# Kernel tuning notes

Measured on AMD Instinct MI355X. Metric: run time of the kernel, lower is better.

Reference implementation:

```python
import jax, jax.numpy as jnp
import numpy as np

B, H, W, C, WS, SHIFT, NH = 64, 14, 14, 1024, 7, 3, 32
HD = C // NH
SCALE = HD ** -0.5

def _rel_index():
    coords = np.stack(np.meshgrid(np.arange(WS), np.arange(WS), indexing='ij'))  # [2,ws,ws]
    flat = coords.reshape(2, -1)
    rel = (flat[:, :, None] - flat[:, None, :]).transpose(1, 2, 0)  # [49,49,2]
    rel[:, :, 0] += WS - 1
    rel[:, :, 1] += WS - 1
    rel[:, :, 0] *= 2 * WS - 1
    return jnp.asarray(rel.sum(-1))  # [49,49] int

REL_IDX = _rel_index()

def _shift_mask():
    m = np.zeros((H, W), np.float32)
    cnt = 0
    for hs in (slice(0, -WS), slice(-WS, -SHIFT), slice(-SHIFT, None)):
        for ws_ in (slice(0, -WS), slice(-WS, -SHIFT), slice(-SHIFT, None)):
            m[hs, ws_] = cnt
            cnt += 1
    mw = m.reshape(H // WS, WS, W // WS, WS).transpose(0, 2, 1, 3).reshape(-1, WS * WS)
    diff = mw[:, None, :] - mw[:, :, None]
    return jnp.asarray(np.where(diff != 0, -100.0, 0.0).astype(np.float32))  # [nW,49,49]

ATTN_MASK = _shift_mask()

def layernorm(x, g, b, eps=1e-5):
    mu = x.mean(-1, keepdims=True)
    var = ((x - mu) ** 2).mean(-1, keepdims=True)
    return (x - mu) * jax.lax.rsqrt(var + eps) * g + b

def window_partition(x):  # [B,H,W,C] -> [B*nW, 49, C]
    x = x.reshape(B, H // WS, WS, W // WS, WS, C)
    return x.transpose(0, 1, 3, 2, 4, 5).reshape(-1, WS * WS, C)

def window_reverse(x):  # [B*nW, 49, C] -> [B,H,W,C]
    x = x.reshape(B, H // WS, W // WS, WS, WS, C)
    return x.transpose(0, 1, 3, 2, 4, 5).reshape(B, H, W, C)

def swin_block(x, p, shift):
    (ln1_g, ln1_b, qkv_w, qkv_b, rpb, proj_w, proj_b,
     ln2_g, ln2_b, fc1_w, fc1_b, fc2_w, fc2_b) = p
    h = layernorm(x, ln1_g, ln1_b).reshape(B, H, W, C)
    if shift:
        h = jnp.roll(h, (-SHIFT, -SHIFT), axis=(1, 2))
    hw = window_partition(h)                              # [Bn,49,C]
    qkv = hw @ qkv_w + qkv_b                              # [Bn,49,3C]
    q, k, v = qkv.reshape(-1, WS * WS, 3, NH, HD).transpose(2, 0, 3, 1, 4)  # each [Bn,NH,49,HD]
    attn = jnp.einsum('bhqd,bhkd->bhqk', q * SCALE, k)    # [Bn,NH,49,49]
    attn = attn + rpb[REL_IDX].transpose(2, 0, 1)[None]   # fused rel-pos bias
    if shift:
        nW = ATTN_MASK.shape[0]
        attn = attn.reshape(B, nW, NH, WS * WS, WS * WS) + ATTN_MASK[None, :, None]
        attn = attn.reshape(-1, NH, WS * WS, WS * WS)
    attn = jax.nn.softmax(attn, axis=-1)
    o = jnp.einsum('bhqk,bhkd->bhqd', attn, v).transpose(0, 2, 1, 3).reshape(-1, WS * WS, C)
    o = o @ proj_w + proj_b
    o = window_reverse(o)
    if shift:
        o = jnp.roll(o, (SHIFT, SHIFT), axis=(1, 2))
    x = x + o.reshape(B, H * W, C)
    h2 = layernorm(x, ln2_g, ln2_b)
    return x + jax.nn.gelu(h2 @ fc1_w + fc1_b, approximate=False) @ fc2_w + fc2_b

def setup_inputs() -> dict:
    key = jax.random.key(0)
    ks = iter(jax.random.split(key, 64))
    def rnd(shape, s=0.02):
        return jax.random.normal(next(ks), shape, jnp.float32) * s
    inp = {'x': jax.random.normal(next(ks), (B, H * W, C), jnp.float32)}
    for i in range(2):
        inp[f'b{i}_ln1_g'] = jnp.ones((C,), jnp.float32)
        inp[f'b{i}_ln1_b'] = jnp.zeros((C,), jnp.float32)
        inp[f'b{i}_qkv_w'] = rnd((C, 3 * C))
        inp[f'b{i}_qkv_b'] = jnp.zeros((3 * C,), jnp.float32)
        inp[f'b{i}_rpb'] = rnd(((2 * WS - 1) ** 2, NH))
        inp[f'b{i}_proj_w'] = rnd((C, C))
        inp[f'b{i}_proj_b'] = jnp.zeros((C,), jnp.float32)
        inp[f'b{i}_ln2_g'] = jnp.ones((C,), jnp.float32)
        inp[f'b{i}_ln2_b'] = jnp.zeros((C,), jnp.float32)
        inp[f'b{i}_fc1_w'] = rnd((C, 4 * C))
        inp[f'b{i}_fc1_b'] = jnp.zeros((4 * C,), jnp.float32)
        inp[f'b{i}_fc2_w'] = rnd((4 * C, C))
        inp[f'b{i}_fc2_b'] = jnp.zeros((C,), jnp.float32)
    inp['h_ln_g'] = jnp.ones((C,), jnp.float32)
    inp['h_ln_b'] = jnp.zeros((C,), jnp.float32)
    inp['h_w1'] = rnd((C, 512)); inp['h_b1'] = jnp.zeros((512,), jnp.float32)
    inp['h_w2'] = rnd((512, 128)); inp['h_b2'] = jnp.zeros((128,), jnp.float32)
    inp['h_w3'] = rnd((128, 2)); inp['h_b3'] = jnp.zeros((2,), jnp.float32)
    return inp

def reference(x,
              b0_ln1_g, b0_ln1_b, b0_qkv_w, b0_qkv_b, b0_rpb, b0_proj_w, b0_proj_b,
              b0_ln2_g, b0_ln2_b, b0_fc1_w, b0_fc1_b, b0_fc2_w, b0_fc2_b,
              b1_ln1_g, b1_ln1_b, b1_qkv_w, b1_qkv_b, b1_rpb, b1_proj_w, b1_proj_b,
              b1_ln2_g, b1_ln2_b, b1_fc1_w, b1_fc1_b, b1_fc2_w, b1_fc2_b,
              h_ln_g, h_ln_b, h_w1, h_b1, h_w2, h_b2, h_w3, h_b3):
    p0 = (b0_ln1_g, b0_ln1_b, b0_qkv_w, b0_qkv_b, b0_rpb, b0_proj_w, b0_proj_b,
          b0_ln2_g, b0_ln2_b, b0_fc1_w, b0_fc1_b, b0_fc2_w, b0_fc2_b)
    p1 = (b1_ln1_g, b1_ln1_b, b1_qkv_w, b1_qkv_b, b1_rpb, b1_proj_w, b1_proj_b,
          b1_ln2_g, b1_ln2_b, b1_fc1_w, b1_fc1_b, b1_fc2_w, b1_fc2_b)
    x = swin_block(x, p0, shift=False)
    x = swin_block(x, p1, shift=True)
    pooled = x.mean(axis=1)  # global avg pool -> [B, C]
    h = layernorm(pooled, h_ln_g, h_ln_b)
    h = jax.nn.gelu(h @ h_w1 + h_b1, approximate=False)  # dropout is identity (eval)
    h = jax.nn.gelu(h @ h_w2 + h_b2, approximate=False)
    return h @ h_w3 + h_b3  # [B, num_classes]
```

## Files before the change

kernel.cpp:

```cpp
#include <hip/hip_runtime.h>
#include <hip/hip_bf16.h>
#include <hip/hip_fp16.h>
#include <math.h>

#define BB 64
#define CC 1024
#define NH 32
#define NTOK (BB * 14 * 14)
#define SCALE 0.17677669529663687f

typedef __attribute__((ext_vector_type(8))) short short8;
typedef __attribute__((ext_vector_type(8))) unsigned short us8;
typedef __attribute__((ext_vector_type(4))) float f32x4;

__device__ __align__(16) float  g_X  [(size_t)NTOK * CC];
__device__ __align__(16) unsigned short g_Qh[(size_t)NTOK * 3072];
__device__ __align__(16) unsigned short g_B[(size_t)NTOK * CC];
__device__ __align__(16) unsigned short g_C[(size_t)NTOK * 4096];
__device__ __align__(16) unsigned short g_Wq[(size_t)2*3072*1024];
__device__ __align__(16) unsigned short g_Wp[(size_t)2*1024*1024];
__device__ __align__(16) unsigned short g_W1[(size_t)2*4096*1024];
__device__ __align__(16) unsigned short g_W2[(size_t)2*1024*4096];
__device__ __align__(16) float g_H0[64 * CC];
__device__ __align__(16) float g_H1[64 * 512];
__device__ __align__(16) float g_H2[64 * 128];

__device__ __forceinline__ float gelu_f(float x) {
    return 0.5f * x * (1.0f + erff(x * 0.70710678118654752f));
}

__device__ __forceinline__ unsigned short f16_bits(float v) {
    _Float16 hh = (_Float16)v;
    return *(unsigned short*)&hh;
}
__device__ __forceinline__ float f16_val(unsigned short u) {
    _Float16 h;
    __builtin_memcpy(&h, &u, 2);
    return (float)h;
}

__device__ __forceinline__ int win_to_xrow(int r, int shifted) {
    int bn = r / 49, t = r - bn * 49;
    int b = bn >> 2, w = bn & 3;
    int wh = w >> 1, ww_ = w & 1;
    int th = t / 7, tw = t - th * 7;
    int gh = wh * 7 + th, gw = ww_ * 7 + tw;
    if (shifted) { gh = gh + 3; if (gh >= 14) gh -= 14; gw = gw + 3; if (gw >= 14) gw -= 14; }
    return b * 196 + gh * 14 + gw;
}

__device__ __forceinline__ void gload_lds16(const void* g, void* l) {
    __builtin_amdgcn_global_load_lds(
        (const __attribute__((address_space(1))) unsigned int*)g,
        (__attribute__((address_space(3))) unsigned int*)l, 16, 0, 0);
}

__global__ __launch_bounds__(256) void convw_kernel(const float* __restrict__ W,
    unsigned short* __restrict__ Wh, int K, int N)
{
    __shared__ float t[32][33];
    int n0 = blockIdx.x * 32, k0 = blockIdx.y * 32;
    int tx = threadIdx.x & 31, ty = threadIdx.x >> 5;
    #pragma unroll
    for (int i = 0; i < 4; ++i)
        t[ty + 8 * i][tx] = W[(size_t)(k0 + ty + 8 * i) * N + n0 + tx];
    __syncthreads();
    #pragma unroll
    for (int i = 0; i < 4; ++i) {
        int n = ty + 8 * i;
        Wh[(size_t)(n0 + n) * K + k0 + tx] = f16_bits(t[tx][n]);
    }
}

__global__ __launch_bounds__(256) void ln_kernel(const float* __restrict__ X,
    const float* __restrict__ g, const float* __restrict__ bta,
    unsigned short* __restrict__ outh, int shifted, int partition)
{
    int token = blockIdx.x * 4 + (threadIdx.x >> 6);
    int lane = threadIdx.x & 63;
    int xrow = partition ? win_to_xrow(token, shifted) : token;
    const float4* src = (const float4*)(X + (size_t)xrow * CC);
    float4 v[4];
    float s = 0.f;
    #pragma unroll
    for (int w = 0; w < 4; ++w) {
        v[w] = src[w * 64 + lane];
        s += v[w].x + v[w].y + v[w].z + v[w].w;
    }
    #pragma unroll
    for (int o = 32; o; o >>= 1) s += __shfl_xor(s, o);
    float mean = s * (1.0f / CC);
    float ss = 0.f;
    #pragma unroll
    for (int w = 0; w < 4; ++w) {
        float d0 = v[w].x - mean, d1 = v[w].y - mean, d2 = v[w].z - mean, d3 = v[w].w - mean;
        ss += d0 * d0 + d1 * d1 + d2 * d2 + d3 * d3;
    }
    #pragma unroll
    for (int o = 32; o; o >>= 1) ss += __shfl_xor(ss, o);
    float inv = 1.0f / sqrtf(ss * (1.0f / CC) + 1e-5f);
    #pragma unroll
    for (int w = 0; w < 4; ++w) {
        int c4 = w * 64 + lane;
        float4 gv = *(const float4*)(g + c4 * 4);
        float4 bv = *(const float4*)(bta + c4 * 4);
        ushort4 uo;
        uo.x = f16_bits((v[w].x - mean) * inv * gv.x + bv.x);
        uo.y = f16_bits((v[w].y - mean) * inv * gv.y + bv.y);
        uo.z = f16_bits((v[w].z - mean) * inv * gv.z + bv.z);
        uo.w = f16_bits((v[w].w - mean) * inv * gv.w + bv.w);
        *(ushort4*)(outh + (size_t)token * CC + c4 * 4) = uo;
    }
}

template<int EPI>
__global__ __launch_bounds__(512) void gemm_mfma(
    const unsigned short* __restrict__ A, const unsigned short* __restrict__ W,
    const float* __restrict__ bias,
    float* __restrict__ outf, unsigned short* __restrict__ outh,
    int N, int K, int shifted, int NR, int GC)
{
    __shared__ unsigned short sm[24576];
    const int tid = threadIdx.x;
    const int wave = tid >> 6, lane = tid & 63;
    const int wr = wave >> 1, wc = wave & 1;
    const int nb = gridDim.x;
    const int wg = (blockIdx.x & 7) * (nb >> 3) + (blockIdx.x >> 3);
    const int gsz = GC * NR;
    const int grp = wg / gsz;
    const int rem = wg - grp * gsz;
    const int by = rem / GC;
    const int bx = grp * GC + (rem - by * GC);
    const int row0 = by * 256, col0 = bx * 128;
    const int rsel = lane & 15;

    f32x4 acc[4][4] = {};

    const int srow = tid >> 3, sslot = tid & 7;

    for (int k0 = 0; k0 < K; k0 += 64) {
        #pragma unroll
        for (int sub = 0; sub < 4; ++sub) {
            const int row = sub * 64 + srow;
            const int c = sslot ^ (row & 7);
            gload_lds16(A + (size_t)(row0 + row) * K + k0 + c * 8,
                        &sm[sub * 4096 + tid * 8]);
        }
        #pragma unroll
        for (int sub = 0; sub < 2; ++sub) {
            const int row = sub * 64 + srow;
            const int c = sslot ^ (row & 7);
            gload_lds16(W + (size_t)(col0 + row) * K + k0 + c * 8,
                        &sm[16384 + sub * 4096 + tid * 8]);
        }
        __syncthreads();

        #pragma unroll
        for (int kk = 0; kk < 2; ++kk) {
            const int kc8 = kk * 4 + (lane >> 4);
            short8 fa[4], fw[4];
            #pragma unroll
            for (int m = 0; m < 4; ++m) {
                int ra = wr * 64 + m * 16 + rsel;
                fa[m] = *(const short8*)&sm[ra * 64 + ((kc8 ^ (ra & 7)) * 8)];
                int rw = wc * 64 + m * 16 + rsel;
                fw[m] = *(const short8*)&sm[16384 + rw * 64 + ((kc8 ^ (rw & 7)) * 8)];
            }
            #pragma unroll
            for (int m = 0; m < 4; ++m)
                #pragma unroll
                for (int n = 0; n < 4; ++n)
                    acc[m][n] = __builtin_amdgcn_mfma_f32_16x16x32_f16(fa[m], fw[n], acc[m][n], 0, 0, 0);
        }
        __syncthreads();
    }

    const int jrow = lane >> 4;
    if (EPI <= 1) {
        #pragma unroll
        for (int half = 0; half < 2; ++half) {
            __syncthreads();
            if ((wr >> 1) == half) {
                #pragma unroll
                for (int n = 0; n < 4; ++n) {
                    int cl = wc * 64 + n * 16 + rsel;
                    float bv = bias[col0 + cl];
                    #pragma unroll
                    for (int m = 0; m < 4; ++m)
                        #pragma unroll
                        for (int j = 0; j < 4; ++j) {
                            int rl = (wr & 1) * 64 + m * 16 + jrow * 4 + j;
                            float v = acc[m][n][j] + bv;
                            if (EPI == 1) v = gelu_f(v);
                            sm[rl * 132 + cl] = f16_bits(v);
                        }
                }
            }
            __syncthreads();
            const int r = tid >> 2, cb = (tid & 3) * 32;
            unsigned short* dst = outh + (size_t)(row0 + half * 128 + r) * N + col0 + cb;
            const unsigned short* src = &sm[r * 132 + cb];
            #pragma unroll
            for (int i = 0; i < 4; ++i)
                *(us8*)(dst + i * 8) = *(const us8*)(src + i * 8);
        }
    } else {
        float* smf = (float*)sm;
        const int rr = tid >> 3;
        const int cc4 = (tid & 7) * 16;
        #pragma unroll
        for (int q = 0; q < 4; ++q) {
            __syncthreads();
            if (wr == q) {
                #pragma unroll
                for (int n = 0; n < 4; ++n) {
                    const int cl = wc * 64 + n * 16 + rsel;
                    const float bv = bias[col0 + cl];
                    #pragma unroll
                    for (int m = 0; m < 4; ++m)
                        #pragma unroll
                        for (int j = 0; j < 4; ++j)
                            smf[(m * 16 + jrow * 4 + j) * 130 + cl] = acc[m][n][j] + bv;
                }
            }
            __syncthreads();
            const int gr = row0 + q * 64 + rr;
            const int orow = (EPI == 2) ? win_to_xrow(gr, shifted) : gr;
            float* dst = outf + (size_t)orow * CC + col0 + cc4;
            const float* srcl = &smf[rr * 130 + cc4];
            #pragma unroll
            for (int i = 0; i < 4; ++i) {
                float4 xv = *(float4*)(dst + i * 4);
                xv.x += srcl[i * 4 + 0];
                xv.y += srcl[i * 4 + 1];
                xv.z += srcl[i * 4 + 2];
                xv.w += srcl[i * 4 + 3];
                *(float4*)(dst + i * 4) = xv;
            }
        }
    }
}

__global__ __launch_bounds__(256) void attn_kernel(const unsigned short* __restrict__ qkv,
    unsigned short* __restrict__ oh, const float* __restrict__ rpb, int shifted)
{
    int blk = blockIdx.x;
    int bn = blk >> 3;
    int hg = blk & 7;
    int wv = threadIdx.x >> 6;
    int lane = threadIdx.x & 63;
    int h = hg * 4 + wv;

    __shared__ float ks[4][49][32], vs[4][49][32];

    for (int idx = lane; idx < 49 * 32; idx += 64) {
        int t = idx >> 5, d = idx & 31;
        const unsigned short* p = qkv + (size_t)(bn * 49 + t) * 3072 + h * 32 + d;
        ks[wv][t][d] = f16_val(p[1024]);
        vs[wv][t][d] = f16_val(p[2048]);
    }
    __syncthreads();

    if (lane < 49) {
        const int i = lane;
        const int ih = i / 7, iw = i - ih * 7;
        const int w = bn & 3, wh = w >> 1, ww_ = w & 1;
        const int gh = wh * 7 + ih, gw = ww_ * 7 + iw;
        const int li = (gh < 7 ? 0 : (gh < 11 ? 1 : 2)) * 3 + (gw < 7 ? 0 : (gw < 11 ? 1 : 2));

        float qreg[32];
        const unsigned short* qp = qkv + (size_t)(bn * 49 + i) * 3072 + h * 32;
        #pragma unroll
        for (int d8 = 0; d8 < 4; ++d8) {
            us8 qv = *(const us8*)(qp + d8 * 8);
            #pragma unroll
            for (int e = 0; e < 8; ++e) {
                unsigned short u = qv[e];
                qreg[d8 * 8 + e] = f16_val(u) * SCALE;
            }
        }

        float p[49];
        float mx = -1e30f;
        #pragma unroll
        for (int j = 0; j < 49; ++j) {
            const int jh = j / 7, jw = j - jh * 7;
            float dot = 0.f;
            #pragma unroll
            for (int d = 0; d < 32; ++d) dot = fmaf(qreg[d], ks[wv][j][d], dot);
            const int ridx = (ih - jh + 6) * 13 + (iw - jw + 6);
            float val = dot + rpb[ridx * 32 + h];
            if (shifted) {
                const int gjh = wh * 7 + jh, gjw = ww_ * 7 + jw;
                const int lj = (gjh < 7 ? 0 : (gjh < 11 ? 1 : 2)) * 3 +
                               (gjw < 7 ? 0 : (gjw < 11 ? 1 : 2));
                if (li != lj) val -= 100.0f;
            }
            p[j] = val;
            mx = fmaxf(mx, val);
        }
        float denom = 0.f;
        #pragma unroll
        for (int j = 0; j < 49; ++j) {
            p[j] = expf(p[j] - mx);
            denom += p[j];
        }
        const float rd = 1.0f / denom;

        unsigned short* orow = oh + (size_t)(bn * 49 + i) * CC + h * 32;
        #pragma unroll 4
        for (int d = 0; d < 32; ++d) {
            float acc = 0.f;
            #pragma unroll
            for (int j = 0; j < 49; ++j) acc = fmaf(p[j], vs[wv][j][d], acc);
            orow[d] = f16_bits(acc * rd);
        }
    }
}

__global__ __launch_bounds__(256) void pool_ln_kernel(const float* __restrict__ X,
    const float* __restrict__ g, const float* __restrict__ bta, float* __restrict__ out)
{
    int b = blockIdx.x, tid = threadIdx.x;
    int lane = tid & 63, wid = tid >> 6;
    const float* base = X + (size_t)b * 196 * CC + tid * 4;
    float a0 = 0, a1 = 0, a2 = 0, a3 = 0;
    for (int t = 0; t < 196; ++t) {
        float4 v = *(const float4*)(base + (size_t)t * CC);
        a0 += v.x; a1 += v.y; a2 += v.z; a3 += v.w;
    }
    const float inv196 = 1.0f / 196.0f;
    float p0 = a0 * inv196, p1 = a1 * inv196, p2 = a2 * inv196, p3 = a3 * inv196;
    float s = p0 + p1 + p2 + p3;
    #pragma unroll
    for (int o = 32; o; o >>= 1) s += __shfl_xor(s, o);
    __shared__ float sred[4], ssred[4];
    if (lane == 0) sred[wid] = s;
    __syncthreads();
    float mean = (sred[0] + sred[1] + sred[2] + sred[3]) * (1.0f / CC);
    float d0 = p0 - mean, d1 = p1 - mean, d2 = p2 - mean, d3 = p3 - mean;
    float ss = d0 * d0 + d1 * d1 + d2 * d2 + d3 * d3;
    #pragma unroll
    for (int o = 32; o; o >>= 1) ss += __shfl_xor(ss, o);
    if (lane == 0) ssred[wid] = ss;
    __syncthreads();
    float var = (ssred[0] + ssred[1] + ssred[2] + ssred[3]) * (1.0f / CC);
    float inv = 1.0f / sqrtf(var + 1e-5f);
    float4 gv = *(const float4*)(g + tid * 4);
    float4 bv = *(const float4*)(bta + tid * 4);
    float4 o4;
    o4.x = d0 * inv * gv.x + bv.x;
    o4.y = d1 * inv * gv.y + bv.y;
    o4.z = d2 * inv * gv.z + bv.z;
    o4.w = d3 * inv * gv.w + bv.w;
    *(float4*)(out + (size_t)b * CC + tid * 4) = o4;
}

__global__ __launch_bounds__(256) void head_rowgemm(const float* __restrict__ A,
    const float* __restrict__ W, const float* __restrict__ bias,
    float* __restrict__ out, int K, int N, int act)
{
    __shared__ float As[1024];
    int r = blockIdx.x, tid = threadIdx.x;
    for (int k = tid; k < K; k += 256) As[k] = A[(size_t)r * K + k];
    __syncthreads();
    for (int c = tid; c < N; c += 256) {
        float s0 = 0.f, s1 = 0.f;
        for (int k = 0; k < K; k += 2) {
            s0 = fmaf(As[k],     W[(size_t)k * N + c],       s0);
            s1 = fmaf(As[k + 1], W[(size_t)(k + 1) * N + c], s1);
        }
        float s = s0 + s1 + bias[c];
        out[(size_t)r * N + c] = act ? gelu_f(s) : s;
    }
}

extern "C" void kernel_launch(void* const* d_in, const int* in_sizes, int n_in,
                              void* d_out, int out_size, void* d_ws, size_t ws_size,
                              hipStream_t stream) {
    const float* x = (const float*)d_in[0];
    auto P = [&](int i) { return (const float*)d_in[i]; };

    float *X, *H0, *H1, *H2;
    unsigned short *QKVh, *B, *C, *Wq, *Wp, *W1, *W2;
    { void* p;
      hipGetSymbolAddress(&p, HIP_SYMBOL(g_X));   X    = (float*)p;
      hipGetSymbolAddress(&p, HIP_SYMBOL(g_Qh));  QKVh = (unsigned short*)p;
      hipGetSymbolAddress(&p, HIP_SYMBOL(g_B));   B    = (unsigned short*)p;
      hipGetSymbolAddress(&p, HIP_SYMBOL(g_C));   C    = (unsigned short*)p;
      hipGetSymbolAddress(&p, HIP_SYMBOL(g_Wq));  Wq   = (unsigned short*)p;
      hipGetSymbolAddress(&p, HIP_SYMBOL(g_Wp));  Wp   = (unsigned short*)p;
      hipGetSymbolAddress(&p, HIP_SYMBOL(g_W1));  W1   = (unsigned short*)p;
      hipGetSymbolAddress(&p, HIP_SYMBOL(g_W2));  W2   = (unsigned short*)p;
      hipGetSymbolAddress(&p, HIP_SYMBOL(g_H0));  H0 = (float*)p;
      hipGetSymbolAddress(&p, HIP_SYMBOL(g_H1));  H1 = (float*)p;
      hipGetSymbolAddress(&p, HIP_SYMBOL(g_H2));  H2 = (float*)p;
    }

    hipMemcpyAsync(X, x, (size_t)NTOK * CC * sizeof(float),
                   hipMemcpyDeviceToDevice, stream);

    for (int blk = 0; blk < 2; ++blk) {
        int base = 1 + blk * 13;
        convw_kernel<<<dim3(3072/32, 1024/32), 256, 0, stream>>>(
            P(base + 2), Wq + (size_t)blk*3072*1024, 1024, 3072);
        convw_kernel<<<dim3(1024/32, 1024/32), 256, 0, stream>>>(
            P(base + 5), Wp + (size_t)blk*1024*1024, 1024, 1024);
        convw_kernel<<<dim3(4096/32, 1024/32), 256, 0, stream>>>(
            P(base + 9), W1 + (size_t)blk*4096*1024, 1024, 4096);
        convw_kernel<<<dim3(1024/32, 4096/32), 256, 0, stream>>>(
            P(base + 11), W2 + (size_t)blk*1024*4096, 4096, 1024);
    }

    for (int blk = 0; blk < 2; ++blk) {
        int base = 1 + blk * 13;
        const float *ln1g = P(base + 0), *ln1b = P(base + 1);
        const float *qkvb = P(base + 3);
        const float *rpb  = P(base + 4);
        const float *projb = P(base + 6);
        const float *ln2g = P(base + 7), *ln2b = P(base + 8);
        const float *fc1b = P(base + 10);
        const float *fc2b = P(base + 12);
        int shifted = blk;
        const unsigned short* wq = Wq + (size_t)blk*3072*1024;
        const unsigned short* wp = Wp + (size_t)blk*1024*1024;
        const unsigned short* w1 = W1 + (size_t)blk*4096*1024;
        const unsigned short* w2 = W2 + (size_t)blk*1024*4096;

        ln_kernel<<<NTOK / 4, 256, 0, stream>>>(X, ln1g, ln1b, B, shifted, 1);
        gemm_mfma<0><<<1176, 512, 0, stream>>>(
            B, wq, qkvb, nullptr, QKVh, 3072, 1024, 0, 49, 8);
        attn_kernel<<<256 * 8, 256, 0, stream>>>(QKVh, B, rpb, shifted);
        gemm_mfma<2><<<392, 512, 0, stream>>>(
            B, wp, projb, X, nullptr, 1024, 1024, shifted, 49, 8);
        ln_kernel<<<NTOK / 4, 256, 0, stream>>>(X, ln2g, ln2b, B, 0, 0);
        gemm_mfma<1><<<1568, 512, 0, stream>>>(
            B, w1, fc1b, nullptr, C, 4096, 1024, 0, 49, 8);
        gemm_mfma<3><<<392, 512, 0, stream>>>(
            C, w2, fc2b, X, nullptr, 1024, 4096, 0, 49, 8);
    }

    pool_ln_kernel<<<64, 256, 0, stream>>>(X, P(27), P(28), H0);
    head_rowgemm<<<64, 256, 0, stream>>>(H0, P(29), P(30), H1, 1024, 512, 1);
    head_rowgemm<<<64, 256, 0, stream>>>(H1, P(31), P(32), H2, 512, 128, 1);
    head_rowgemm<<<64, 256, 0, stream>>>(H2, P(33), P(34), (float*)d_out, 128, 2, 0);
}
```

Baseline: 1.565 ms.

## Double-buffer GEMM K-loop with 256x256 tiles and uneven XCD remap

The MFMA GEMM moves from a 256x128 tile to a 256x256 tile, with each wave now computing 128x64. The K loop is double-buffered in 128KB of LDS: the next K slice is prefetched with direct-to-LDS loads while the current one is consumed, using explicit vmcnt waits and raw barriers. Block-to-XCD remapping now handles grid sizes not divisible by 8, and launch grids are halved to match. This aims to hide global-load latency and raise arithmetic intensity. In exchange, the 256-wide N tile leaves fewer blocks for the N=1024 GEMMs (196 blocks), so occupancy and CU fill drop.

Result: slower. 1.782 ms (+13.9%).

```diff
diff --git a/kernel.cpp b/kernel.cpp
--- a/kernel.cpp
+++ b/kernel.cpp
@@ -114,122 +114,149 @@
 }
 
 template<int EPI>
-__global__ __launch_bounds__(512) void gemm_mfma(
+__global__ __launch_bounds__(512, 2) void gemm_mfma(
     const unsigned short* __restrict__ A, const unsigned short* __restrict__ W,
     const float* __restrict__ bias,
     float* __restrict__ outf, unsigned short* __restrict__ outh,
     int N, int K, int shifted, int NR, int GC)
 {
-    __shared__ unsigned short sm[24576];
+    __shared__ unsigned short sm[65536];
     const int tid = threadIdx.x;
     const int wave = tid >> 6, lane = tid & 63;
-    const int wr = wave >> 1, wc = wave & 1;
-    const int nb = gridDim.x;
-    const int wg = (blockIdx.x & 7) * (nb >> 3) + (blockIdx.x >> 3);
+    const int wm = wave >> 2, wn = wave & 3;
+    const int nb = gridDim.x, bid = blockIdx.x;
+    const int q8 = nb >> 3, r8 = nb & 7;
+    const int xcd = bid & 7, idx = bid >> 3;
+    const int wg = (xcd < r8 ? xcd * (q8 + 1) : r8 * (q8 + 1) + (xcd - r8) * q8) + idx;
     const int gsz = GC * NR;
     const int grp = wg / gsz;
     const int rem = wg - grp * gsz;
     const int by = rem / GC;
     const int bx = grp * GC + (rem - by * GC);
-    const int row0 = by * 256, col0 = bx * 128;
+    const int row0 = by * 256, col0 = bx * 256;
     const int rsel = lane & 15;
-
-    f32x4 acc[4][4] = {};
-
-    const int srow = tid >> 3, sslot = tid & 7;
-
-    for (int k0 = 0; k0 < K; k0 += 64) {
-        #pragma unroll
-        for (int sub = 0; sub < 4; ++sub) {
-            const int row = sub * 64 + srow;
-            const int c = sslot ^ (row & 7);
-            gload_lds16(A + (size_t)(row0 + row) * K + k0 + c * 8,
-                        &sm[sub * 4096 + tid * 8]);
-        }
-        #pragma unroll
-        for (int sub = 0; sub < 2; ++sub) {
-            const int row = sub * 64 + srow;
-            const int c = sslot ^ (row & 7);
-            gload_lds16(W + (size_t)(col0 + row) * K + k0 + c * 8,
-                        &sm[16384 + sub * 4096 + tid * 8]);
-        }
-        __syncthreads();
-
+    const int jrow = lane >> 4;
+
+    f32x4 acc[8][4] = {};
+
+    auto STAGE = [&](int tt) {
+        const int base = (tt & 1) << 15;
+        const int k0 = tt << 6;
+        #pragma unroll
+        for (int s = 0; s < 4; ++s) {
+            const int qq = s * 512 + tid;
+            const int row = qq >> 3;
+            const int kc = (qq & 7) ^ (row & 7);
+            gload_lds16(A + (size_t)(row0 + row) * K + k0 + kc * 8,
+                        &sm[base + qq * 8]);
+        }
+        #pragma unroll
+        for (int s = 0; s < 4; ++s) {
+            const int qq = s * 512 + tid;
+            const int row = qq >> 3;
+            const int kc = (qq & 7) ^ (row & 7);
+            gload_lds16(W + (size_t)(col0 + row) * K + k0 + kc * 8,
+                        &sm[base + 16384 + qq * 8]);
+        }
+    };
+
+    const int nt = K >> 6;
+    STAGE(0);
+    for (int t = 0; t < nt; ++t) {
+        if (t > 0) {
+            __builtin_amdgcn_s_barrier();
+            __builtin_amdgcn_sched_barrier(0);
+        }
+        if (t + 1 < nt) {
+            STAGE(t + 1);
+            __builtin_amdgcn_sched_barrier(0);
+            asm volatile("s_waitcnt vmcnt(8)" ::: "memory");
+        } else {
+            asm volatile("s_waitcnt vmcnt(0)" ::: "memory");
+        }
+        __builtin_amdgcn_sched_barrier(0);
+        __builtin_amdgcn_s_barrier();
+        __builtin_amdgcn_sched_barrier(0);
+
+        const int bb = (t & 1) << 15;
         #pragma unroll
         for (int kk = 0; kk < 2; ++kk) {
-            const int kc8 = kk * 4 + (lane >> 4);
-            short8 fa[4], fw[4];
-            #pragma unroll
-            for (int m = 0; m < 4; ++m) {
-                int ra = wr * 64 + m * 16 + rsel;
-                fa[m] = *(const short8*)&sm[ra * 64 + ((kc8 ^ (ra & 7)) * 8)];
-                int rw = wc * 64 + m * 16 + rsel;
-                fw[m] = *(const short8*)&sm[16384 + rw * 64 + ((kc8 ^ (rw & 7)) * 8)];
-            }
-            #pragma unroll
-            for (int m = 0; m < 4; ++m)
+            const int kx = ((kk * 4 + (lane >> 4)) ^ (rsel & 7)) * 8;
+            short8 fa[8], fw[4];
+            #pragma unroll
+            for (int m = 0; m < 8; ++m) {
+                const int ra = wm * 128 + m * 16 + rsel;
+                fa[m] = *(const short8*)&sm[bb + ra * 64 + kx];
+            }
+            #pragma unroll
+            for (int n = 0; n < 4; ++n) {
+                const int rw = wn * 64 + n * 16 + rsel;
+                fw[n] = *(const short8*)&sm[bb + 16384 + rw * 64 + kx];
+            }
+            #pragma unroll
+            for (int m = 0; m < 8; ++m)
                 #pragma unroll
                 for (int n = 0; n < 4; ++n)
                     acc[m][n] = __builtin_amdgcn_mfma_f32_16x16x32_f16(fa[m], fw[n], acc[m][n], 0, 0, 0);
         }
-        __syncthreads();
-    }
-
-    const int jrow = lane >> 4;
+    }
+
     if (EPI <= 1) {
         #pragma unroll
-        for (int half = 0; half < 2; ++half) {
+        for (int h = 0; h < 2; ++h) {
             __syncthreads();
-            if ((wr >> 1) == half) {
+            if (wm == h) {
                 #pragma unroll
                 for (int n = 0; n < 4; ++n) {
-                    int cl = wc * 64 + n * 16 + rsel;
-                    float bv = bias[col0 + cl];
+                    const int cl = wn * 64 + n * 16 + rsel;
+                    const float bv = bias[col0 + cl];
                     #pragma unroll
-                    for (int m = 0; m < 4; ++m)
+                    for (int m = 0; m < 8; ++m)
                         #pragma unroll
                         for (int j = 0; j < 4; ++j) {
-                            int rl = (wr & 1) * 64 + m * 16 + jrow * 4 + j;
+                            const int rl = m * 16 + jrow * 4 + j;
                             float v = acc[m][n][j] + bv;
                             if (EPI == 1) v = gelu_f(v);
-                            sm[rl * 132 + cl] = f16_bits(v);
+                            sm[rl * 264 + cl] = f16_bits(v);
                         }
                 }
             }
             __syncthreads();
-            const int r = tid >> 2, cb = (tid & 3) * 32;
-            unsigned short* dst = outh + (size_t)(row0 + half * 128 + r) * N + col0 + cb;
-            const unsigned short* src = &sm[r * 132 + cb];
-            #pragma unroll
-            for (int i = 0; i < 4; ++i)
+            const int r = tid >> 2, cb = (tid & 3) * 64;
+            unsigned short* dst = outh + (size_t)(row0 + h * 128 + r) * N + col0 + cb;
+            const unsigned short* src = &sm[r * 264 + cb];
+            #pragma unroll
+            for (int i = 0; i < 8; ++i)
                 *(us8*)(dst + i * 8) = *(const us8*)(src + i * 8);
         }
     } else {
         float* smf = (float*)sm;
-        const int rr = tid >> 3;
-        const int cc4 = (tid & 7) * 16;
-        #pragma unroll
-        for (int q = 0; q < 4; ++q) {
+        #pragma unroll
+        for (int qq = 0; qq < 4; ++qq) {
             __syncthreads();
-            if (wr == q) {
+            if (wm == (qq >> 1)) {
+                const int mlo = (qq & 1) * 4;
                 #pragma unroll
                 for (int n = 0; n < 4; ++n) {
-                    const int cl = wc * 64 + n * 16 + rsel;
+                    const int cl = wn * 64 + n * 16 + rsel;
                     const float bv = bias[col0 + cl];
                     #pragma unroll
-                    for (int m = 0; m < 4; ++m)
+                    for (int mi = 0; mi < 4; ++mi)
                         #pragma unroll
                         for (int j = 0; j < 4; ++j)
-                            smf[(m * 16 + jrow * 4 + j) * 130 + cl] = acc[m][n][j] + bv;
+                            smf[(mi * 16 + jrow * 4 + j) * 260 + cl] =
+                                acc[mlo + mi][n][j] + bv;
                 }
             }
             __syncthreads();
-            const int gr = row0 + q * 64 + rr;
+            const int rr = tid >> 3;
+            const int c0 = (tid & 7) * 32;
+            const int gr = row0 + qq * 64 + rr;
             const int orow = (EPI == 2) ? win_to_xrow(gr, shifted) : gr;
-            float* dst = outf + (size_t)orow * CC + col0 + cc4;
-            const float* srcl = &smf[rr * 130 + cc4];
-            #pragma unroll
-            for (int i = 0; i < 4; ++i) {
+            float* dst = outf + (size_t)orow * CC + col0 + c0;
+            const float* srcl = &smf[rr * 260 + c0];
+            #pragma unroll
+            for (int i = 0; i < 8; ++i) {
                 float4 xv = *(float4*)(dst + i * 4);
                 xv.x += srcl[i * 4 + 0];
                 xv.y += srcl[i * 4 + 1];
@@ -428,16 +455,16 @@
         const unsigned short* w2 = W2 + (size_t)blk*1024*4096;
 
         ln_kernel<<<NTOK / 4, 256, 0, stream>>>(X, ln1g, ln1b, B, shifted, 1);
-        gemm_mfma<0><<<1176, 512, 0, stream>>>(
-            B, wq, qkvb, nullptr, QKVh, 3072, 1024, 0, 49, 8);
+        gemm_mfma<0><<<588, 512, 0, stream>>>(
+            B, wq, qkvb, nullptr, QKVh, 3072, 1024, 0, 49, 4);
         attn_kernel<<<256 * 8, 256, 0, stream>>>(QKVh, B, rpb, shifted);
-        gemm_mfma<2><<<392, 512, 0, stream>>>(
-            B, wp, projb, X, nullptr, 1024, 1024, shifted, 49, 8);
+        gemm_mfma<2><<<196, 512, 0, stream>>>(
+            B, wp, projb, X, nullptr, 1024, 1024, shifted, 49, 4);
         ln_kernel<<<NTOK / 4, 256, 0, stream>>>(X, ln2g, ln2b, B, 0, 0);
-        gemm_mfma<1><<<1568, 512, 0, stream>>>(
+        gemm_mfma<1><<<784, 512, 0, stream>>>(
             B, w1, fc1b, nullptr, C, 4096, 1024, 0, 49, 8);
-        gemm_mfma<3><<<392, 512, 0, stream>>>(
-            C, w2, fc2b, X, nullptr, 1024, 4096, 0, 49, 8);
+        gemm_mfma<3><<<196, 512, 0, stream>>>(
+            C, w2, fc2b, X, nullptr, 1024, 4096, 0, 49, 4);
     }
 
     pool_ln_kernel<<<64, 256, 0, stream>>>(X, P(27), P(28), H0);
```
